# Kernel tuning notes

Hardware: AMD Instinct MI355X
Metric: run time of the kernel (lower is better)

The kernel has to match this reference:

```python
import math
import jax, jax.numpy as jnp
import numpy as np

B, N, DIM, E, G, TOPK, DEPTH = 64, 512, 128, 16, 32, 4, 1
HID = 4 * DIM
EPS = 1e-8
LAMBDA_INIT = 0.8 - 0.6 * math.exp(-0.3 * DEPTH)


def setup_inputs() -> dict:
    key = jax.random.key(0)
    ks = jax.random.split(key, 16)
    d = {}
    d["x"] = jax.random.normal(ks[0], (B, N, DIM), jnp.float32)
    d["bias"] = jnp.zeros((1,), jnp.float32)
    d["attn_scale"] = jnp.ones((DIM,), jnp.float32)
    d["ffn_scale"] = jnp.ones((DIM,), jnp.float32)
    d["Wr"] = jax.random.normal(ks[1], (DIM, E), jnp.float32) * 0.05
    d["br"] = jnp.zeros((E,), jnp.float32)
    d["E1"] = jax.random.uniform(ks[2], (2, E, N, G), jnp.float32)
    d["E2"] = jax.random.uniform(ks[3], (2, E, G, N), jnp.float32)
    d["lambda_q1"] = jax.random.normal(ks[4], (DIM,), jnp.float32) * 0.1
    d["lambda_k1"] = jax.random.normal(ks[5], (DIM,), jnp.float32) * 0.1
    d["lambda_q2"] = jax.random.normal(ks[6], (DIM,), jnp.float32) * 0.1
    d["lambda_k2"] = jax.random.normal(ks[7], (DIM,), jnp.float32) * 0.1
    d["outer_lambda"] = jnp.log(jnp.asarray(99.0, jnp.float32))
    d["W1"] = jax.random.normal(ks[8], (DIM, HID), jnp.float32) * 0.02
    d["b1"] = jnp.zeros((HID,), jnp.float32)
    d["W2"] = jax.random.normal(ks[9], (DIM, HID), jnp.float32) * 0.02
    d["b2"] = jnp.zeros((HID,), jnp.float32)
    d["W3"] = jax.random.normal(ks[10], (HID, DIM), jnp.float32) * 0.02
    d["b3"] = jnp.zeros((DIM,), jnp.float32)
    return d


def _rmsnorm(v, scale):
    # RMSNorm with p<0: full L2 norm over last dim, rms = ||v|| / sqrt(d)
    rms = jnp.linalg.norm(v, axis=-1, keepdims=True) * (DIM ** -0.5)
    return scale * (v / (rms + EPS))


def reference(x, bias, attn_scale, ffn_scale, Wr, br, E1, E2,
              lambda_q1, lambda_k1, lambda_q2, lambda_k2, outer_lambda,
              W1, b1, W2, b2, W3, b3):
    # ---- pre-norm ----
    xn = _rmsnorm(x, attn_scale)                       # [B,N,F]

    # ---- top-k routing (selector) ----
    route_logits = xn @ Wr + br                        # [B,N,E]
    gate = jax.nn.sigmoid(route_logits)
    _, topk_idx = jax.lax.top_k(gate + bias, TOPK)     # [B,N,K]
    mask = jnp.sum(jax.nn.one_hot(topk_idx, E, dtype=gate.dtype), axis=-2)  # [B,N,E]
    # sigmoid(route + log(mask)) == sigmoid(route) * mask (mask in {0,1})
    gated = gate * mask
    route = gated / jnp.sum(gated, axis=-1, keepdims=True)

    # ---- coefficient: concat([1], -(exp(q1.k1) - exp(q2.k2) + lambda_init)) ----
    l1 = jnp.exp(jnp.sum(lambda_q1 * lambda_k1))
    l2 = jnp.exp(jnp.sum(lambda_q2 * lambda_k2))
    lambda_full = -(l1 - l2 + LAMBDA_INIT)
    coef = jnp.concatenate([jnp.ones((1,), x.dtype), lambda_full[None]])  # [2]

    # ---- outer mixing matrix (convex comb of eye with itself -> eye, kept faithful) ----
    w = jax.nn.sigmoid(outer_lambda)
    eye = jnp.eye(DIM, dtype=x.dtype)
    outer = w * eye + (1.0 - w) * eye                  # [F,F]

    # ---- expert graph mixing: bik,e,ekid,ekdj,bjf,fc->bic ----
    A1 = jax.nn.softmax(E1, axis=-1)                   # [2,E,N,G]
    A2 = jax.nn.softmax(E2, axis=-1)                   # [2,E,G,N]
    M = jnp.einsum('ekid,ekdj->ekij', A1, A2)          # [2,E,N,N]
    s = jnp.einsum('bik,ekij->beij', route, M)         # [B,2,N,N]
    xc = jnp.einsum('bjf,fc->bjc', xn, outer)          # [B,N,F]
    attn = jnp.einsum('e,beij,bjc->bic', coef, s, xc)  # [B,N,F]

    x = x + attn

    # ---- SwiGLU FFN (dropout is identity at inference) ----
    xn2 = _rmsnorm(x, ffn_scale)
    h = jax.nn.silu(xn2 @ W1 + b1) * (xn2 @ W2 + b2)   # [B,N,4F]
    x = x + h @ W3 + b3
    return x, topk_idx
```

## Files before the change

### kernel.cpp

```cpp
#include <hip/hip_runtime.h>
#include <math.h>

#define B_ 64
#define N_ 512
#define DIM_ 128
#define E_ 16
#define G_ 32
#define TOPK_ 4
#define HID_ 512

constexpr int BN_ROWS = B_ * N_;

using bf16x8 = __attribute__((ext_vector_type(8))) short;
using s16x4  = __attribute__((ext_vector_type(4))) short;
using f32x4  = __attribute__((ext_vector_type(4))) float;

__device__ __forceinline__ float bf2f(short s) {
    union { unsigned u; float f; } x;
    x.u = ((unsigned)(unsigned short)s) << 16;
    return x.f;
}
__device__ __forceinline__ short f2bf(float f) {
    union { float f; unsigned u; } x;
    x.f = f;
    unsigned r = x.u + 0x7FFF + ((x.u >> 16) & 1);
    return (short)(r >> 16);
}

__device__ __forceinline__ bf16x8 frag_ld(const short* base, int row, int ks, int lhi) {
    int addr = row * 128 + (((ks * 64) + lhi * 16) ^ ((row & 7) << 4));
    return *(const bf16x8*)((const char*)base + addr);
}

typedef __attribute__((address_space(3))) void lds_vt;
typedef __attribute__((address_space(1))) const void gbl_vt;
__device__ __forceinline__ void gl2lds(const void* g, void* l) {
    __builtin_amdgcn_global_load_lds((gbl_vt*)g, (lds_vt*)l, 16, 0, 0);
}
__device__ __forceinline__ void vm0_bar() {
    asm volatile("s_waitcnt vmcnt(0)" ::: "memory");
    __builtin_amdgcn_sched_barrier(0);
    __builtin_amdgcn_s_barrier();
    __builtin_amdgcn_sched_barrier(0);
}
__device__ __forceinline__ void lgkm0_bar() {
    asm volatile("s_waitcnt lgkmcnt(0)" ::: "memory");
    __builtin_amdgcn_sched_barrier(0);
    __builtin_amdgcn_s_barrier();
    __builtin_amdgcn_sched_barrier(0);
}

constexpr int NPRE = BN_ROWS / 4;
constexpr int NXNT = B_ * 16;
constexpr int NSMG = 32 * 512 / 8;
constexpr int NSMN = 1024 / 4;
constexpr int NTW  = 64 * 3;
constexpr int NMISC = NPRE + NXNT + NSMG + NSMN + NTW + 1;

__global__ __launch_bounds__(256) void k_misc(
    const float* __restrict__ x, const float* __restrict__ attn_s,
    const float* __restrict__ Wr, const float* __restrict__ br, const float* __restrict__ bias,
    float* __restrict__ route, float* __restrict__ topk_out,
    short* __restrict__ xnT,
    const float* __restrict__ E1, short* __restrict__ A1nb,
    const float* __restrict__ E2, short* __restrict__ A2nb,
    const float* __restrict__ W1, const float* __restrict__ W2, const float* __restrict__ W3,
    short* __restrict__ W1T, short* __restrict__ W2T, short* __restrict__ W3T,
    const float* __restrict__ lq1, const float* __restrict__ lk1,
    const float* __restrict__ lq2, const float* __restrict__ lk2,
    float lam_init, float* __restrict__ lam_out) {
    __shared__ float tb[32][129];
    __shared__ float invb[32];
    __shared__ float tw[32][33];
    int blk = blockIdx.x;
    int tid = threadIdx.x;

    if (blk < NPRE) {
        int w = tid >> 6, lane = tid & 63;
        int row = blk * 4 + w;
        float2 v = ((const float2*)(x + (size_t)row * DIM_))[lane];
        float ss = v.x * v.x + v.y * v.y;
        for (int off = 32; off; off >>= 1) ss += __shfl_xor(ss, off);
        float inv = 1.0f / (sqrtf(ss * (1.0f / DIM_)) + 1e-8f);
        float2 s = ((const float2*)attn_s)[lane];
        float xn0 = v.x * inv * s.x;
        float xn1 = v.y * inv * s.y;
        int e = lane & 15, chunk = lane >> 4;
        float acc = 0.f;
#pragma unroll
        for (int j = 0; j < 16; ++j) {
            int srcl = chunk * 16 + j;
            float a0 = __shfl(xn0, srcl);
            float a1 = __shfl(xn1, srcl);
            int d0 = chunk * 32 + 2 * j;
            acc += a0 * Wr[d0 * E_ + e] + a1 * Wr[(d0 + 1) * E_ + e];
        }
        acc += __shfl_xor(acc, 16);
        acc += __shfl_xor(acc, 32);
        float gate = 1.0f / (1.0f + expf(-(acc + br[e])));
        float vv = gate + bias[0];
        int rank = 0;
#pragma unroll
        for (int i = 0; i < 16; ++i) {
            float vi = __shfl(vv, i);
            rank += ((vi > vv) || (vi == vv && i < e)) ? 1 : 0;
        }
        bool selq = (rank < TOPK_) && (lane < 16);
        float contrib = selq ? gate : 0.f;
        float ssum = contrib;
        ssum += __shfl_xor(ssum, 1); ssum += __shfl_xor(ssum, 2);
        ssum += __shfl_xor(ssum, 4); ssum += __shfl_xor(ssum, 8);
        if (lane < 16) route[(size_t)row * E_ + e] = selq ? gate / ssum : 0.0f;
        if (selq) topk_out[(size_t)row * TOPK_ + rank] = (float)e;
        return;
    }
    blk -= NPRE;

    if (blk < NXNT) {
        int b = blk >> 4, j0 = (blk & 15) * 32;
        const float* src = x + (size_t)(b * 512 + j0) * 128;
        int r = tid >> 3, c8 = tid & 7;
#pragma unroll
        for (int it = 0; it < 4; ++it) {
            int c4 = c8 + it * 8;
            float4 w4 = *(const float4*)(src + (size_t)r * 128 + c4 * 4);
            tb[r][c4 * 4 + 0] = w4.x; tb[r][c4 * 4 + 1] = w4.y;
            tb[r][c4 * 4 + 2] = w4.z; tb[r][c4 * 4 + 3] = w4.w;
        }
        __syncthreads();
        int sg = tid & 7;
        float ps = 0.f;
#pragma unroll
        for (int j = 0; j < 16; ++j) { float e2 = tb[r][sg * 16 + j]; ps += e2 * e2; }
        ps += __shfl_xor(ps, 1); ps += __shfl_xor(ps, 2); ps += __shfl_xor(ps, 4);
        if (sg == 0) invb[r] = 1.0f / (sqrtf(ps * (1.0f / DIM_)) + 1e-8f);
        __syncthreads();
        int c = tid >> 1, half = tid & 1;
        float sc = attn_s[c];
        short ov[16];
#pragma unroll
        for (int j = 0; j < 16; ++j) {
            int jj = half * 16 + j;
            ov[j] = f2bf(tb[jj][c] * invb[jj] * sc);
        }
        short* dst = xnT + (size_t)(b * 128 + c) * 512 + j0 + half * 16;
        *(bf16x8*)dst = *(bf16x8*)ov;
        *(bf16x8*)(dst + 8) = *(bf16x8*)(ov + 8);
        return;
    }
    blk -= NXNT;

    if (blk < NSMG) {
        int row = blk * 8 + (tid >> 5);
        int l = tid & 31;
        float v = E1[(size_t)row * 32 + l];
        float m = v;
        for (int off = 16; off; off >>= 1) m = fmaxf(m, __shfl_xor(m, off));
        float ev = expf(v - m);
        float s = ev;
        for (int off = 16; off; off >>= 1) s += __shfl_xor(s, off);
        A1nb[(size_t)row * 32 + l] = f2bf(ev / s);
        return;
    }
    blk -= NSMG;

    if (blk < NSMN) {
        int row = blk * 4 + (tid >> 6);
        int l = tid & 63;
        const float* p = E2 + (size_t)row * 512;
        float v[8];
        float m = -1e30f;
#pragma unroll
        for (int j = 0; j < 8; ++j) { v[j] = p[l + j * 64]; m = fmaxf(m, v[j]); }
        for (int off = 32; off; off >>= 1) m = fmaxf(m, __shfl_xor(m, off));
        float s = 0.f;
#pragma unroll
        for (int j = 0; j < 8; ++j) { v[j] = expf(v[j] - m); s += v[j]; }
        for (int off = 32; off; off >>= 1) s += __shfl_xor(s, off);
        float inv = 1.0f / s;
        short* q = A2nb + (size_t)row * 512;
#pragma unroll
        for (int j = 0; j < 8; ++j) q[l + j * 64] = f2bf(v[j] * inv);
        return;
    }
    blk -= NSMN;

    if (blk < NTW) {
        int m = blk >> 6, tile = blk & 63;
        const float* S = (m == 0) ? W1 : (m == 1) ? W2 : W3;
        short* D = (m == 0) ? W1T : (m == 1) ? W2T : W3T;
        int R = (m == 2) ? 512 : 128, C = (m == 2) ? 128 : 512;
        int ctiles = C / 32;
        int r0 = (tile / ctiles) * 32, c0 = (tile % ctiles) * 32;
        int tx = tid & 31, ty = tid >> 5;
#pragma unroll
        for (int r = 0; r < 4; ++r) tw[ty * 4 + r][tx] = S[(size_t)(r0 + ty * 4 + r) * C + c0 + tx];
        __syncthreads();
#pragma unroll
        for (int r = 0; r < 4; ++r) D[(size_t)(c0 + ty * 4 + r) * R + r0 + tx] = f2bf(tw[tx][ty * 4 + r]);
        return;
    }

    if (tid < 64) {
        int l = tid;
        float s1 = lq1[l] * lk1[l] + lq1[l + 64] * lk1[l + 64];
        float s2 = lq2[l] * lk2[l] + lq2[l + 64] * lk2[l + 64];
        for (int off = 32; off; off >>= 1) {
            s1 += __shfl_xor(s1, off);
            s2 += __shfl_xor(s2, off);
        }
        if (l == 0) lam_out[0] = -(expf(s1) - expf(s2) + lam_init);
    }
}

__global__ __launch_bounds__(256) void k_gemm_y(const short* __restrict__ A2nb,
                                                const short* __restrict__ xnT,
                                                short* __restrict__ YT) {
    alignas(16) __shared__ short As0[128 * 64];
    alignas(16) __shared__ short Bs0[128 * 64];
    alignas(16) __shared__ short As1[128 * 64];
    alignas(16) __shared__ short Bs1[128 * 64];
    int id = blockIdx.x;
    int nid = ((id & 7) << 6) + (id >> 3);
    int m0 = (nid & 3) * 128;
    int be = nid >> 2, b = be >> 1, e = be & 1;
    int tid = threadIdx.x, lane = tid & 63, wid = tid >> 6;
    int l15 = lane & 15, lhi = lane >> 4;
    int wr = wid >> 1, wc = wid & 1;
    const short* Asrc = A2nb + (size_t)e * 512 * 512 + (size_t)m0 * 512;
    const short* Bsrc = xnT + (size_t)b * 128 * 512;
    int row8 = lane >> 3;
    int chunk8 = (lane & 7) ^ row8;

    auto stage = [&](short* Ad, short* Bd, int k0) {
#pragma unroll
        for (int t = 0; t < 4; ++t) {
            int i = wid * 4 + t;
            int row = i * 8 + row8;
            gl2lds(Asrc + (size_t)row * 512 + k0 + chunk8 * 8, (char*)Ad + i * 1024);
            gl2lds(Bsrc + (size_t)row * 512 + k0 + chunk8 * 8, (char*)Bd + i * 1024);
        }
    };
    f32x4 acc[4][4] = {};
    stage(As0, Bs0, 0);
    for (int s = 0; s < 8; ++s) {
        vm0_bar();
        const short* Ac = (s & 1) ? As1 : As0;
        const short* Bc = (s & 1) ? Bs1 : Bs0;
        if (s < 7) stage((s & 1) ? As0 : As1, (s & 1) ? Bs0 : Bs1, (s + 1) * 64);
#pragma unroll
        for (int ks = 0; ks < 2; ++ks) {
            bf16x8 af[4], bfr[4];
#pragma unroll
            for (int i = 0; i < 4; ++i) af[i] = frag_ld(Ac, wr * 64 + i * 16 + l15, ks, lhi);
#pragma unroll
            for (int j = 0; j < 4; ++j) bfr[j] = frag_ld(Bc, wc * 64 + j * 16 + l15, ks, lhi);
#pragma unroll
            for (int i = 0; i < 4; ++i)
#pragma unroll
                for (int j = 0; j < 4; ++j)
                    acc[i][j] = __builtin_amdgcn_mfma_f32_16x16x32_bf16(af[i], bfr[j], acc[i][j], 0, 0, 0);
        }
    }
    short* Yb = YT + (size_t)b * 128 * 1024 + e * 512;
#pragma unroll
    for (int i = 0; i < 4; ++i) {
        int mbase = m0 + wr * 64 + i * 16 + lhi * 4;
#pragma unroll
        for (int j = 0; j < 4; ++j) {
            int n = wc * 64 + j * 16 + l15;
            s16x4 o;
#pragma unroll
            for (int q = 0; q < 4; ++q) o[q] = f2bf(acc[i][j][q]);
            *(s16x4*)(Yb + (size_t)n * 1024 + mbase) = o;
        }
    }
}

__global__ __launch_bounds__(256) void k_attn(const short* __restrict__ A1nb,
                                              const float* __restrict__ route,
                                              const short* __restrict__ YT,
                                              const float* __restrict__ x,
                                              const float* __restrict__ lam_p,
                                              const float* __restrict__ ffn_s,
                                              float* __restrict__ x1,
                                              short* __restrict__ xn2b) {
    alignas(16) __shared__ short Ab0[64 * 64];
    alignas(16) __shared__ short Ab1[64 * 64];
    alignas(16) __shared__ short Bb0[128 * 64];
    alignas(16) __shared__ short Bb1[128 * 64];
    __shared__ float ssbuf[2][64];
    int id = blockIdx.x;
    int nid = ((id & 7) << 6) + (id >> 3);
    int m0 = (nid & 7) * 64;
    int b = nid >> 3;
    float lam = lam_p[0];
    int tid = threadIdx.x, lane = tid & 63, wid = tid >> 6;
    int l15 = lane & 15, lhi = lane >> 4;
    int wr = wid >> 1, wc = wid & 1;
    const short* YTb = YT + (size_t)b * 128 * 1024;
    int row8 = lane >> 3;
    int chunk8 = (lane & 7) ^ row8;

    auto stageB = [&](short* Bd, int k0) {
#pragma unroll
        for (int t = 0; t < 4; ++t) {
            int i = wid * 4 + t;
            int row = i * 8 + row8;
            gl2lds(YTb + (size_t)row * 1024 + k0 + chunk8 * 8, (char*)Bd + i * 1024);
        }
    };
    auto loadA = [&](float (&rv)[2], bf16x8 (&ar)[2], int sn) {
#pragma unroll
        for (int r = 0; r < 2; ++r) {
            int idx = tid + r * 256, rowl = idx >> 3, slot = idx & 7;
            int t = sn * 2 + (slot >> 2);
            int gi = m0 + rowl;
            rv[r] = route[((size_t)b * 512 + gi) * 16 + (t & 15)] * (t >= 16 ? lam : 1.0f);
            ar[r] = *(const bf16x8*)(A1nb + ((size_t)t * 512 + gi) * 32 + (slot & 3) * 8);
        }
    };
    auto writeA = [&](short* dst, float (&rv)[2], bf16x8 (&ar)[2]) {
#pragma unroll
        for (int r = 0; r < 2; ++r) {
            int idx = tid + r * 256, rowl = idx >> 3, slot = idx & 7;
            bf16x8 o;
#pragma unroll
            for (int q = 0; q < 8; ++q) o[q] = f2bf(bf2f(ar[r][q]) * rv[r]);
            *(bf16x8*)((char*)dst + rowl * 128 + ((slot * 16) ^ ((rowl & 7) << 4))) = o;
        }
    };
    f32x4 acc[2][4] = {};
    auto compute = [&](const short* Ac, const short* Bc) {
#pragma unroll
        for (int ks = 0; ks < 2; ++ks) {
            bf16x8 af[2], bfr[4];
#pragma unroll
            for (int i = 0; i < 2; ++i) af[i] = frag_ld(Ac, wr * 32 + i * 16 + l15, ks, lhi);
#pragma unroll
            for (int j = 0; j < 4; ++j) bfr[j] = frag_ld(Bc, wc * 64 + j * 16 + l15, ks, lhi);
#pragma unroll
            for (int i = 0; i < 2; ++i)
#pragma unroll
                for (int j = 0; j < 4; ++j)
                    acc[i][j] = __builtin_amdgcn_mfma_f32_16x16x32_bf16(af[i], bfr[j], acc[i][j], 0, 0, 0);
        }
    };

    float rv0[2], rv1[2];
    bf16x8 ar0[2], ar1[2];
    stageB(Bb0, 0);
    loadA(rv0, ar0, 0);
    for (int sp = 0; sp < 8; ++sp) {
        int s = sp * 2;
        vm0_bar();
        stageB(Bb1, (s + 1) * 64);
        loadA(rv1, ar1, s + 1);
        writeA(Ab0, rv0, ar0);
        lgkm0_bar();
        compute(Ab0, Bb0);
        vm0_bar();
        if (s + 2 < 16) {
            stageB(Bb0, (s + 2) * 64);
            loadA(rv0, ar0, s + 2);
        }
        writeA(Ab1, rv1, ar1);
        lgkm0_bar();
        compute(Ab1, Bb1);
    }
    float x1v[2][4][4];
    float pss[2][4] = {};
#pragma unroll
    for (int i = 0; i < 2; ++i) {
        int gibase = m0 + wr * 32 + i * 16 + lhi * 4;
#pragma unroll
        for (int j = 0; j < 4; ++j) {
            int n = wc * 64 + j * 16 + l15;
#pragma unroll
            for (int q = 0; q < 4; ++q) {
                size_t off = ((size_t)b * 512 + gibase + q) * 128 + n;
                float val = acc[i][j][q] + x[off];
                x1[off] = val;
                x1v[i][j][q] = val;
                pss[i][q] += val * val;
            }
        }
    }
#pragma unroll
    for (int i = 0; i < 2; ++i)
#pragma unroll
        for (int q = 0; q < 4; ++q) {
            float p = pss[i][q];
            p += __shfl_xor(p, 1); p += __shfl_xor(p, 2);
            p += __shfl_xor(p, 4); p += __shfl_xor(p, 8);
            pss[i][q] = p;
        }
    if (l15 == 0) {
#pragma unroll
        for (int i = 0; i < 2; ++i)
#pragma unroll
            for (int q = 0; q < 4; ++q)
                ssbuf[wc][wr * 32 + i * 16 + lhi * 4 + q] = pss[i][q];
    }
    __syncthreads();
#pragma unroll
    for (int i = 0; i < 2; ++i)
#pragma unroll
        for (int q = 0; q < 4; ++q) {
            int rowl = wr * 32 + i * 16 + lhi * 4 + q;
            float ssum = ssbuf[0][rowl] + ssbuf[1][rowl];
            float inv = 1.0f / (sqrtf(ssum * (1.0f / DIM_)) + 1e-8f);
#pragma unroll
            for (int j = 0; j < 4; ++j) {
                int n = wc * 64 + j * 16 + l15;
                xn2b[((size_t)b * 512 + m0 + rowl) * 128 + n] = f2bf(x1v[i][j][q] * inv * ffn_s[n]);
            }
        }
}

__global__ __launch_bounds__(256) void k_ffn1(const short* __restrict__ xn2b,
                                              const short* __restrict__ W1T, const float* __restrict__ b1,
                                              const short* __restrict__ W2T, const float* __restrict__ b2,
                                              short* __restrict__ h) {
    alignas(16) __shared__ short As0[128 * 64];
    alignas(16) __shared__ short B10[64 * 64];
    alignas(16) __shared__ short B20[64 * 64];
    alignas(16) __shared__ short As1[128 * 64];
    alignas(16) __shared__ short B11[64 * 64];
    alignas(16) __shared__ short B21[64 * 64];
    int id = blockIdx.x;
    int nid = ((id & 7) << 8) + (id >> 3);
    int n0 = (nid & 7) * 64;
    int m0 = (nid >> 3) * 128;
    int tid = threadIdx.x, lane = tid & 63, wid = tid >> 6;
    int l15 = lane & 15, lhi = lane >> 4;
    int wr = wid >> 1, wc = wid & 1;
    int row8 = lane >> 3;
    int chunk8 = (lane & 7) ^ row8;

    auto stage = [&](short* Ad, short* B1d, short* B2d, int k0) {
#pragma unroll
        for (int t = 0; t < 8; ++t) {
            int i = wid * 8 + t;
            if (i < 16) {
                int row = i * 8 + row8;
                gl2lds(xn2b + (size_t)(m0 + row) * 128 + k0 + chunk8 * 8, (char*)Ad + i * 1024);
            } else if (i < 24) {
                int ii = i - 16, row = ii * 8 + row8;
                gl2lds(W1T + (size_t)(n0 + row) * 128 + k0 + chunk8 * 8, (char*)B1d + ii * 1024);
            } else {
                int ii = i - 24, row = ii * 8 + row8;
                gl2lds(W2T + (size_t)(n0 + row) * 128 + k0 + chunk8 * 8, (char*)B2d + ii * 1024);
            }
        }
    };
    f32x4 acc1[4][2] = {}, acc2[4][2] = {};
    stage(As0, B10, B20, 0);
    for (int s = 0; s < 2; ++s) {
        vm0_bar();
        const short* Ac = s ? As1 : As0;
        const short* B1c = s ? B11 : B10;
        const short* B2c = s ? B21 : B20;
        if (s == 0) stage(As1, B11, B21, 64);
#pragma unroll
        for (int ks = 0; ks < 2; ++ks) {
            bf16x8 af[4], b1f[2], b2f[2];
#pragma unroll
            for (int i = 0; i < 4; ++i) af[i] = frag_ld(Ac, wr * 64 + i * 16 + l15, ks, lhi);
#pragma unroll
            for (int j = 0; j < 2; ++j) {
                b1f[j] = frag_ld(B1c, wc * 32 + j * 16 + l15, ks, lhi);
                b2f[j] = frag_ld(B2c, wc * 32 + j * 16 + l15, ks, lhi);
            }
#pragma unroll
            for (int i = 0; i < 4; ++i)
#pragma unroll
                for (int j = 0; j < 2; ++j) {
                    acc1[i][j] = __builtin_amdgcn_mfma_f32_16x16x32_bf16(af[i], b1f[j], acc1[i][j], 0, 0, 0);
                    acc2[i][j] = __builtin_amdgcn_mfma_f32_16x16x32_bf16(af[i], b2f[j], acc2[i][j], 0, 0, 0);
                }
        }
    }
    __syncthreads();
#pragma unroll
    for (int i = 0; i < 4; ++i) {
        int mloc = wr * 64 + i * 16 + lhi * 4;
#pragma unroll
        for (int j = 0; j < 2; ++j) {
            int nloc = wc * 32 + j * 16 + l15;
            int n = n0 + nloc;
            float bb1 = b1[n], bb2 = b2[n];
#pragma unroll
            for (int q = 0; q < 4; ++q) {
                float a1 = acc1[i][j][q] + bb1;
                float a2 = acc2[i][j][q] + bb2;
                float hv = a1 / (1.0f + expf(-a1)) * a2;
                ((short*)As0)[(mloc + q) * 64 + nloc] = f2bf(hv);
            }
        }
    }
    __syncthreads();
#pragma unroll
    for (int r = 0; r < 4; ++r) {
        int idx = tid + r * 256;
        int row = idx >> 3, slot = idx & 7;
        *(bf16x8*)(h + (size_t)(m0 + row) * 512 + n0 + slot * 8) =
            *(const bf16x8*)((char*)As0 + row * 128 + slot * 16);
    }
}

__global__ __launch_bounds__(256) void k_ffn2(const short* __restrict__ h,
                                              const short* __restrict__ W3T, const float* __restrict__ b3,
                                              const float* __restrict__ x1,
                                              float* __restrict__ out) {
    alignas(16) __shared__ short As0[64 * 64];
    alignas(16) __shared__ short Bs0[128 * 64];
    alignas(16) __shared__ short As1[64 * 64];
    alignas(16) __shared__ short Bs1[128 * 64];
    int m0 = blockIdx.x * 64;
    int tid = threadIdx.x, lane = tid & 63, wid = tid >> 6;
    int l15 = lane & 15, lhi = lane >> 4;
    int wr = wid >> 1, wc = wid & 1;
    int row8 = lane >> 3;
    int chunk8 = (lane & 7) ^ row8;

    auto stage = [&](short* Ad, short* Bd, int k0) {
#pragma unroll
        for (int t = 0; t < 6; ++t) {
            int i = wid * 6 + t;
            if (i < 8) {
                int row = i * 8 + row8;
                gl2lds(h + (size_t)(m0 + row) * 512 + k0 + chunk8 * 8, (char*)Ad + i * 1024);
            } else {
                int ii = i - 8, row = ii * 8 + row8;
                gl2lds(W3T + (size_t)row * 512 + k0 + chunk8 * 8, (char*)Bd + ii * 1024);
            }
        }
    };
    f32x4 acc[2][4] = {};
    stage(As0, Bs0, 0);
    for (int s = 0; s < 8; ++s) {
        vm0_bar();
        const short* Ac = (s & 1) ? As1 : As0;
        const short* Bc = (s & 1) ? Bs1 : Bs0;
        if (s < 7) stage((s & 1) ? As0 : As1, (s & 1) ? Bs0 : Bs1, (s + 1) * 64);
#pragma unroll
        for (int ks = 0; ks < 2; ++ks) {
            bf16x8 af[2], bfr[4];
#pragma unroll
            for (int i = 0; i < 2; ++i) af[i] = frag_ld(Ac, wr * 32 + i * 16 + l15, ks, lhi);
#pragma unroll
            for (int j = 0; j < 4; ++j) bfr[j] = frag_ld(Bc, wc * 64 + j * 16 + l15, ks, lhi);
#pragma unroll
            for (int i = 0; i < 2; ++i)
#pragma unroll
                for (int j = 0; j < 4; ++j)
                    acc[i][j] = __builtin_amdgcn_mfma_f32_16x16x32_bf16(af[i], bfr[j], acc[i][j], 0, 0, 0);
        }
    }
#pragma unroll
    for (int i = 0; i < 2; ++i) {
        int mbase = m0 + wr * 32 + i * 16 + lhi * 4;
#pragma unroll
        for (int j = 0; j < 4; ++j) {
            int n = wc * 64 + j * 16 + l15;
            float bv = b3[n];
#pragma unroll
            for (int q = 0; q < 4; ++q) {
                size_t off = (size_t)(mbase + q) * 128 + n;
                out[off] = acc[i][j][q] + x1[off] + bv;
            }
        }
    }
}

constexpr size_t ALIGN_UP(size_t x) { return (x + 255) & ~(size_t)255; }
constexpr size_t SZ_X1   = ALIGN_UP((size_t)BN_ROWS * DIM_ * 4);
constexpr size_t SZ_RT   = ALIGN_UP((size_t)BN_ROWS * E_ * 4);
constexpr size_t SZ_A1   = ALIGN_UP((size_t)32 * 512 * 32 * 2);
constexpr size_t SZ_A2   = ALIGN_UP((size_t)2 * 512 * 512 * 2);
constexpr size_t SZ_XNT  = ALIGN_UP((size_t)B_ * 128 * 512 * 2);
constexpr size_t SZ_YT   = ALIGN_UP((size_t)B_ * 128 * 1024 * 2);
constexpr size_t SZ_XN2B = ALIGN_UP((size_t)BN_ROWS * DIM_ * 2);
constexpr size_t SZ_H    = ALIGN_UP((size_t)BN_ROWS * HID_ * 2);
constexpr size_t SZ_WT   = ALIGN_UP((size_t)128 * 512 * 2);

extern "C" void kernel_launch(void* const* d_in, const int* in_sizes, int n_in,
                              void* d_out, int out_size, void* d_ws, size_t ws_size,
                              hipStream_t stream) {
    const float* x      = (const float*)d_in[0];
    const float* bias   = (const float*)d_in[1];
    const float* attn_s = (const float*)d_in[2];
    const float* ffn_s  = (const float*)d_in[3];
    const float* Wr     = (const float*)d_in[4];
    const float* br     = (const float*)d_in[5];
    const float* E1     = (const float*)d_in[6];
    const float* E2     = (const float*)d_in[7];
    const float* lq1    = (const float*)d_in[8];
    const float* lk1    = (const float*)d_in[9];
    const float* lq2    = (const float*)d_in[10];
    const float* lk2    = (const float*)d_in[11];
    const float* W1     = (const float*)d_in[13];
    const float* b1     = (const float*)d_in[14];
    const float* W2     = (const float*)d_in[15];
    const float* b2     = (const float*)d_in[16];
    const float* W3     = (const float*)d_in[17];
    const float* b3     = (const float*)d_in[18];

    char* p = (char*)d_ws;
    float* x1   = (float*)p;            p += SZ_X1;
    float* rt   = (float*)p;            p += SZ_RT;
    short* A1nb = (short*)p;            p += SZ_A1;
    short* A2nb = (short*)p;            p += SZ_A2;
    short* xnT  = (short*)p;            p += SZ_XNT;
    short* YT   = (short*)p;            p += SZ_YT;
    short* xn2b = (short*)p;            p += SZ_XN2B;
    short* h    = (short*)p;            p += SZ_H;
    short* W1T  = (short*)p;            p += SZ_WT;
    short* W2T  = (short*)p;            p += SZ_WT;
    short* W3T  = (short*)p;            p += SZ_WT;
    float* lam  = (float*)p;            p += 256;

    float* out_x   = (float*)d_out;
    float* out_idx = out_x + (size_t)BN_ROWS * DIM_;

    float lam_init = 0.8f - 0.6f * expf(-0.3f);

    hipLaunchKernelGGL(k_misc, dim3(NMISC), dim3(256), 0, stream,
                       x, attn_s, Wr, br, bias, rt, out_idx, xnT,
                       E1, A1nb, E2, A2nb, W1, W2, W3, W1T, W2T, W3T,
                       lq1, lk1, lq2, lk2, lam_init, lam);
    hipLaunchKernelGGL(k_gemm_y, dim3(512), dim3(256), 0, stream, A2nb, xnT, YT);
    hipLaunchKernelGGL(k_attn, dim3(512), dim3(256), 0, stream, A1nb, rt, YT, x, lam, ffn_s, x1, xn2b);
    hipLaunchKernelGGL(k_ffn1, dim3(2048), dim3(256), 0, stream, xn2b, W1T, b1, W2T, b2, h);
    hipLaunchKernelGGL(k_ffn2, dim3(512), dim3(256), 0, stream, h, W3T, b3, x1, out_x);
}
```

Baseline: 203.7 us.

## Fuse SwiGLU FFN kernels and relax vmcnt waits in GEMM pipelines

Merges the two FFN kernels into one per-row-tile kernel that computes each 64-wide hidden chunk into LDS and immediately accumulates it against W3, so the bf16 hidden tensor never goes to global memory. Separately, the double-buffered loops in k_gemm_y and k_attn now wait only on the older batch of loads (vmcnt 8) instead of all loads, with extra barriers added so the next prefetch can overlap compute. The fused kernel runs the W1/W2 and W3 phases serially with full waits, and its 512-block grid with heavy LDS use may limit occupancy and latency hiding.

```diff
diff --git a/kernel.cpp b/kernel.cpp
--- a/kernel.cpp
+++ b/kernel.cpp
@@ -31,14 +31,19 @@
     int addr = row * 128 + (((ks * 64) + lhi * 16) ^ ((row & 7) << 4));
     return *(const bf16x8*)((const char*)base + addr);
 }
+__device__ __forceinline__ bf16x8 frag_ld128(const short* base, int row, int ks, int lhi) {
+    int addr = row * 256 + (((ks * 64) + lhi * 16) ^ ((row & 7) << 4));
+    return *(const bf16x8*)((const char*)base + addr);
+}
 
 typedef __attribute__((address_space(3))) void lds_vt;
 typedef __attribute__((address_space(1))) const void gbl_vt;
 __device__ __forceinline__ void gl2lds(const void* g, void* l) {
     __builtin_amdgcn_global_load_lds((gbl_vt*)g, (lds_vt*)l, 16, 0, 0);
 }
-__device__ __forceinline__ void vm0_bar() {
-    asm volatile("s_waitcnt vmcnt(0)" ::: "memory");
+#define WAIT_VMCNT(N) do { asm volatile("s_waitcnt vmcnt(" #N ")" ::: "memory"); \
+    __builtin_amdgcn_sched_barrier(0); } while (0)
+__device__ __forceinline__ void barrier_() {
     __builtin_amdgcn_sched_barrier(0);
     __builtin_amdgcn_s_barrier();
     __builtin_amdgcn_sched_barrier(0);
@@ -244,10 +249,15 @@
     f32x4 acc[4][4] = {};
     stage(As0, Bs0, 0);
     for (int s = 0; s < 8; ++s) {
-        vm0_bar();
         const short* Ac = (s & 1) ? As1 : As0;
         const short* Bc = (s & 1) ? Bs1 : Bs0;
-        if (s < 7) stage((s & 1) ? As0 : As1, (s & 1) ? Bs0 : Bs1, (s + 1) * 64);
+        if (s < 7) {
+            stage((s & 1) ? As0 : As1, (s & 1) ? Bs0 : Bs1, (s + 1) * 64);
+            WAIT_VMCNT(8);
+        } else {
+            WAIT_VMCNT(0);
+        }
+        barrier_();
 #pragma unroll
         for (int ks = 0; ks < 2; ++ks) {
             bf16x8 af[4], bfr[4];
@@ -261,6 +271,7 @@
                 for (int j = 0; j < 4; ++j)
                     acc[i][j] = __builtin_amdgcn_mfma_f32_16x16x32_bf16(af[i], bfr[j], acc[i][j], 0, 0, 0);
         }
+        barrier_();
     }
     short* Yb = YT + (size_t)b * 128 * 1024 + e * 512;
 #pragma unroll
@@ -353,20 +364,26 @@
     loadA(rv0, ar0, 0);
     for (int sp = 0; sp < 8; ++sp) {
         int s = sp * 2;
-        vm0_bar();
         stageB(Bb1, (s + 1) * 64);
         loadA(rv1, ar1, s + 1);
+        WAIT_VMCNT(8);
+        barrier_();
         writeA(Ab0, rv0, ar0);
         lgkm0_bar();
         compute(Ab0, Bb0);
-        vm0_bar();
+        barrier_();
         if (s + 2 < 16) {
             stageB(Bb0, (s + 2) * 64);
             loadA(rv0, ar0, s + 2);
-        }
+            WAIT_VMCNT(8);
+        } else {
+            WAIT_VMCNT(0);
+        }
+        barrier_();
         writeA(Ab1, rv1, ar1);
         lgkm0_bar();
         compute(Ab1, Bb1);
+        barrier_();
     }
     float x1v[2][4][4];
     float pss[2][4] = {};
@@ -418,144 +435,127 @@
         }
 }
 
-__global__ __launch_bounds__(256) void k_ffn1(const short* __restrict__ xn2b,
-                                              const short* __restrict__ W1T, const float* __restrict__ b1,
-                                              const short* __restrict__ W2T, const float* __restrict__ b2,
-                                              short* __restrict__ h) {
-    alignas(16) __shared__ short As0[128 * 64];
-    alignas(16) __shared__ short B10[64 * 64];
-    alignas(16) __shared__ short B20[64 * 64];
-    alignas(16) __shared__ short As1[128 * 64];
-    alignas(16) __shared__ short B11[64 * 64];
-    alignas(16) __shared__ short B21[64 * 64];
+__global__ __launch_bounds__(256) void k_ffn(const short* __restrict__ xn2b,
+                                             const short* __restrict__ W1T, const float* __restrict__ b1,
+                                             const short* __restrict__ W2T, const float* __restrict__ b2,
+                                             const short* __restrict__ W3T, const float* __restrict__ b3,
+                                             const float* __restrict__ x1,
+                                             float* __restrict__ out) {
+    alignas(16) __shared__ short Xs[64 * 128];
+    alignas(16) __shared__ short Hs[64 * 64];
+    alignas(16) __shared__ short W1s[64 * 128];
+    alignas(16) __shared__ short W2s[64 * 128];
+    alignas(16) __shared__ short W3s[128 * 64];
     int id = blockIdx.x;
-    int nid = ((id & 7) << 8) + (id >> 3);
-    int n0 = (nid & 7) * 64;
-    int m0 = (nid >> 3) * 128;
+    int nid = ((id & 7) << 6) + (id >> 3);
+    int m0 = nid * 64;
     int tid = threadIdx.x, lane = tid & 63, wid = tid >> 6;
     int l15 = lane & 15, lhi = lane >> 4;
     int wr = wid >> 1, wc = wid & 1;
-    int row8 = lane >> 3;
-    int chunk8 = (lane & 7) ^ row8;
-
-    auto stage = [&](short* Ad, short* B1d, short* B2d, int k0) {
+
+    int r4 = lane >> 4;
+    int c16 = lane & 15;
+    int r8 = lane >> 3;
+    int c8 = lane & 7;
+
+    auto stageX = [&]() {
+#pragma unroll
+        for (int t = 0; t < 4; ++t) {
+            int i = wid * 4 + t;
+            int row = i * 4 + r4;
+            int cs = c16 ^ (row & 7);
+            gl2lds(xn2b + (size_t)(m0 + row) * 128 + cs * 8, (char*)Xs + i * 1024);
+        }
+    };
+    auto stageW12 = [&](int p) {
+        int n0 = p * 64;
 #pragma unroll
         for (int t = 0; t < 8; ++t) {
             int i = wid * 8 + t;
-            if (i < 16) {
-                int row = i * 8 + row8;
-                gl2lds(xn2b + (size_t)(m0 + row) * 128 + k0 + chunk8 * 8, (char*)Ad + i * 1024);
-            } else if (i < 24) {
-                int ii = i - 16, row = ii * 8 + row8;
-                gl2lds(W1T + (size_t)(n0 + row) * 128 + k0 + chunk8 * 8, (char*)B1d + ii * 1024);
-            } else {
-                int ii = i - 24, row = ii * 8 + row8;
-                gl2lds(W2T + (size_t)(n0 + row) * 128 + k0 + chunk8 * 8, (char*)B2d + ii * 1024);
+            int which = i >> 4;
+            int ii = i & 15;
+            int row = ii * 4 + r4;
+            int cs = c16 ^ (row & 7);
+            const short* S = which ? W2T : W1T;
+            short* D = which ? (short*)W2s : (short*)W1s;
+            gl2lds(S + (size_t)(n0 + row) * 128 + cs * 8, (char*)D + ii * 1024);
+        }
+    };
+    auto stageW3 = [&](int p) {
+        int n0 = p * 64;
+#pragma unroll
+        for (int t = 0; t < 4; ++t) {
+            int i = wid * 4 + t;
+            int row = i * 8 + r8;
+            int cs = c8 ^ (row & 7);
+            gl2lds(W3T + (size_t)row * 512 + n0 + cs * 8, (char*)W3s + i * 1024);
+        }
+    };
+
+    f32x4 aout[2][4] = {};
+    stageX();
+    stageW12(0);
+    stageW3(0);
+    WAIT_VMCNT(0);
+    barrier_();
+    for (int p = 0; p < 8; ++p) {
+        f32x4 a1[2][2] = {}, a2[2][2] = {};
+#pragma unroll
+        for (int ks = 0; ks < 4; ++ks) {
+            bf16x8 af[2], b1f[2], b2f[2];
+#pragma unroll
+            for (int i = 0; i < 2; ++i) af[i] = frag_ld128(Xs, wr * 32 + i * 16 + l15, ks, lhi);
+#pragma unroll
+            for (int j = 0; j < 2; ++j) {
+                b1f[j] = frag_ld128(W1s, wc * 32 + j * 16 + l15, ks, lhi);
+                b2f[j] = frag_ld128(W2s, wc * 32 + j * 16 + l15, ks, lhi);
             }
-        }
-    };
-    f32x4 acc1[4][2] = {}, acc2[4][2] = {};
-    stage(As0, B10, B20, 0);
-    for (int s = 0; s < 2; ++s) {
-        vm0_bar();
-        const short* Ac = s ? As1 : As0;
-        const short* B1c = s ? B11 : B10;
-        const short* B2c = s ? B21 : B20;
-        if (s == 0) stage(As1, B11, B21, 64);
-#pragma unroll
-        for (int ks = 0; ks < 2; ++ks) {
-            bf16x8 af[4], b1f[2], b2f[2];
-#pragma unroll
-            for (int i = 0; i < 4; ++i) af[i] = frag_ld(Ac, wr * 64 + i * 16 + l15, ks, lhi);
+#pragma unroll
+            for (int i = 0; i < 2; ++i)
+#pragma unroll
+                for (int j = 0; j < 2; ++j) {
+                    a1[i][j] = __builtin_amdgcn_mfma_f32_16x16x32_bf16(af[i], b1f[j], a1[i][j], 0, 0, 0);
+                    a2[i][j] = __builtin_amdgcn_mfma_f32_16x16x32_bf16(af[i], b2f[j], a2[i][j], 0, 0, 0);
+                }
+        }
+        int nn0 = p * 64;
+#pragma unroll
+        for (int i = 0; i < 2; ++i) {
+            int mloc = wr * 32 + i * 16 + lhi * 4;
 #pragma unroll
             for (int j = 0; j < 2; ++j) {
-                b1f[j] = frag_ld(B1c, wc * 32 + j * 16 + l15, ks, lhi);
-                b2f[j] = frag_ld(B2c, wc * 32 + j * 16 + l15, ks, lhi);
+                int nloc = wc * 32 + j * 16 + l15;
+                float bb1 = b1[nn0 + nloc], bb2 = b2[nn0 + nloc];
+#pragma unroll
+                for (int q = 0; q < 4; ++q) {
+                    float u = a1[i][j][q] + bb1;
+                    float w2v = a2[i][j][q] + bb2;
+                    float hv = u / (1.0f + expf(-u)) * w2v;
+                    int mq = mloc + q;
+                    *(short*)((char*)Hs + mq * 128 + ((nloc * 2) ^ ((mq & 7) << 4))) = f2bf(hv);
+                }
             }
-#pragma unroll
-            for (int i = 0; i < 4; ++i)
-#pragma unroll
-                for (int j = 0; j < 2; ++j) {
-                    acc1[i][j] = __builtin_amdgcn_mfma_f32_16x16x32_bf16(af[i], b1f[j], acc1[i][j], 0, 0, 0);
-                    acc2[i][j] = __builtin_amdgcn_mfma_f32_16x16x32_bf16(af[i], b2f[j], acc2[i][j], 0, 0, 0);
-                }
-        }
-    }
-    __syncthreads();
-#pragma unroll
-    for (int i = 0; i < 4; ++i) {
-        int mloc = wr * 64 + i * 16 + lhi * 4;
-#pragma unroll
-        for (int j = 0; j < 2; ++j) {
-            int nloc = wc * 32 + j * 16 + l15;
-            int n = n0 + nloc;
-            float bb1 = b1[n], bb2 = b2[n];
-#pragma unroll
-            for (int q = 0; q < 4; ++q) {
-                float a1 = acc1[i][j][q] + bb1;
-                float a2 = acc2[i][j][q] + bb2;
-                float hv = a1 / (1.0f + expf(-a1)) * a2;
-                ((short*)As0)[(mloc + q) * 64 + nloc] = f2bf(hv);
-            }
-        }
-    }
-    __syncthreads();
-#pragma unroll
-    for (int r = 0; r < 4; ++r) {
-        int idx = tid + r * 256;
-        int row = idx >> 3, slot = idx & 7;
-        *(bf16x8*)(h + (size_t)(m0 + row) * 512 + n0 + slot * 8) =
-            *(const bf16x8*)((char*)As0 + row * 128 + slot * 16);
-    }
-}
-
-__global__ __launch_bounds__(256) void k_ffn2(const short* __restrict__ h,
-                                              const short* __restrict__ W3T, const float* __restrict__ b3,
-                                              const float* __restrict__ x1,
-                                              float* __restrict__ out) {
-    alignas(16) __shared__ short As0[64 * 64];
-    alignas(16) __shared__ short Bs0[128 * 64];
-    alignas(16) __shared__ short As1[64 * 64];
-    alignas(16) __shared__ short Bs1[128 * 64];
-    int m0 = blockIdx.x * 64;
-    int tid = threadIdx.x, lane = tid & 63, wid = tid >> 6;
-    int l15 = lane & 15, lhi = lane >> 4;
-    int wr = wid >> 1, wc = wid & 1;
-    int row8 = lane >> 3;
-    int chunk8 = (lane & 7) ^ row8;
-
-    auto stage = [&](short* Ad, short* Bd, int k0) {
-#pragma unroll
-        for (int t = 0; t < 6; ++t) {
-            int i = wid * 6 + t;
-            if (i < 8) {
-                int row = i * 8 + row8;
-                gl2lds(h + (size_t)(m0 + row) * 512 + k0 + chunk8 * 8, (char*)Ad + i * 1024);
-            } else {
-                int ii = i - 8, row = ii * 8 + row8;
-                gl2lds(W3T + (size_t)row * 512 + k0 + chunk8 * 8, (char*)Bd + ii * 1024);
-            }
-        }
-    };
-    f32x4 acc[2][4] = {};
-    stage(As0, Bs0, 0);
-    for (int s = 0; s < 8; ++s) {
-        vm0_bar();
-        const short* Ac = (s & 1) ? As1 : As0;
-        const short* Bc = (s & 1) ? Bs1 : Bs0;
-        if (s < 7) stage((s & 1) ? As0 : As1, (s & 1) ? Bs0 : Bs1, (s + 1) * 64);
+        }
+        lgkm0_bar();
+        if (p < 7) stageW12(p + 1);
 #pragma unroll
         for (int ks = 0; ks < 2; ++ks) {
             bf16x8 af[2], bfr[4];
 #pragma unroll
-            for (int i = 0; i < 2; ++i) af[i] = frag_ld(Ac, wr * 32 + i * 16 + l15, ks, lhi);
-#pragma unroll
-            for (int j = 0; j < 4; ++j) bfr[j] = frag_ld(Bc, wc * 64 + j * 16 + l15, ks, lhi);
+            for (int i = 0; i < 2; ++i) af[i] = frag_ld(Hs, wr * 32 + i * 16 + l15, ks, lhi);
+#pragma unroll
+            for (int j = 0; j < 4; ++j) bfr[j] = frag_ld(W3s, wc * 64 + j * 16 + l15, ks, lhi);
 #pragma unroll
             for (int i = 0; i < 2; ++i)
 #pragma unroll
                 for (int j = 0; j < 4; ++j)
-                    acc[i][j] = __builtin_amdgcn_mfma_f32_16x16x32_bf16(af[i], bfr[j], acc[i][j], 0, 0, 0);
+                    aout[i][j] = __builtin_amdgcn_mfma_f32_16x16x32_bf16(af[i], bfr[j], aout[i][j], 0, 0, 0);
+        }
+        barrier_();
+        if (p < 7) {
+            stageW3(p + 1);
+            WAIT_VMCNT(0);
+            barrier_();
         }
     }
 #pragma unroll
@@ -568,7 +568,7 @@
 #pragma unroll
             for (int q = 0; q < 4; ++q) {
                 size_t off = (size_t)(mbase + q) * 128 + n;
-                out[off] = acc[i][j][q] + x1[off] + bv;
+                out[off] = aout[i][j][q] + x1[off] + bv;
             }
         }
     }
@@ -582,7 +582,6 @@
 constexpr size_t SZ_XNT  = ALIGN_UP((size_t)B_ * 128 * 512 * 2);
 constexpr size_t SZ_YT   = ALIGN_UP((size_t)B_ * 128 * 1024 * 2);
 constexpr size_t SZ_XN2B = ALIGN_UP((size_t)BN_ROWS * DIM_ * 2);
-constexpr size_t SZ_H    = ALIGN_UP((size_t)BN_ROWS * HID_ * 2);
 constexpr size_t SZ_WT   = ALIGN_UP((size_t)128 * 512 * 2);
 
 extern "C" void kernel_launch(void* const* d_in, const int* in_sizes, int n_in,
@@ -615,7 +614,6 @@
     short* xnT  = (short*)p;            p += SZ_XNT;
     short* YT   = (short*)p;            p += SZ_YT;
     short* xn2b = (short*)p;            p += SZ_XN2B;
-    short* h    = (short*)p;            p += SZ_H;
     short* W1T  = (short*)p;            p += SZ_WT;
     short* W2T  = (short*)p;            p += SZ_WT;
     short* W3T  = (short*)p;            p += SZ_WT;
@@ -632,6 +630,5 @@
                        lq1, lk1, lq2, lk2, lam_init, lam);
     hipLaunchKernelGGL(k_gemm_y, dim3(512), dim3(256), 0, stream, A2nb, xnT, YT);
     hipLaunchKernelGGL(k_attn, dim3(512), dim3(256), 0, stream, A1nb, rt, YT, x, lam, ffn_s, x1, xn2b);
-    hipLaunchKernelGGL(k_ffn1, dim3(2048), dim3(256), 0, stream, xn2b, W1T, b1, W2T, b2, h);
-    hipLaunchKernelGGL(k_ffn2, dim3(512), dim3(256), 0, stream, h, W3T, b3, x1, out_x);
-}
+    hipLaunchKernelGGL(k_ffn, dim3(512), dim3(256), 0, stream, xn2b, W1T, b1, W2T, b2, W3T, b3, x1, out_x);
+}
```

New measurement: 197.1 us. 1.03x faster.
